# Optimization experiments

Measured on AMD Instinct MI355X. Metric: run time of the kernel, lower is better.

## Reference

```python
import jax, jax.numpy as jnp
import numpy as np

N_HEAD = 8
D_HEAD = 64
HIDDEN = 512
T = 2048
BS = 4
SCALE = D_HEAD ** -0.5


def setup_inputs() -> dict:
    key = jax.random.key(0)
    k1, k2, k3 = jax.random.split(key, 3)
    x = jax.random.normal(k1, (BS, T, HIDDEN), dtype=jnp.float32)
    # torch Linear weight is (out,in); we store as (in,out) for x @ W
    W_qkv = jax.random.normal(k2, (HIDDEN, (2 * N_HEAD + 1) * D_HEAD), dtype=jnp.float32) * 0.02
    W_out = jax.random.normal(k3, (D_HEAD, HIDDEN), dtype=jnp.float32) * 0.02
    return {"x": x, "W_qkv": W_qkv, "W_out": W_out}


def reference(x, W_qkv, W_out):
    bs, t, h = x.shape
    qkv = x @ W_qkv  # (bs, t, (2H+1)*d)
    q, k, v = jnp.split(qkv, [N_HEAD * D_HEAD, 2 * N_HEAD * D_HEAD], axis=-1)
    q = q.reshape(bs, t, N_HEAD, D_HEAD)
    k = k.reshape(bs, t, N_HEAD, D_HEAD)
    # v is shared across heads: (bs, t, d)
    score = jnp.einsum("bqhd,bkhd->bhqk", q, k) * SCALE
    causal = jnp.triu(jnp.full((t, t), -jnp.inf, dtype=score.dtype), 1)
    score = score + causal[None, None, :, :]
    prob = jax.nn.softmax(score, axis=-1)  # (bs, H, t, t)
    attn_vec = jnp.einsum("bhqk,bkd->bhqd", prob, v)  # shared V broadcast over heads
    m_attn_vec = jnp.mean(attn_vec, axis=1)  # head-mean: (bs, t, d)
    out = m_attn_vec @ W_out  # (bs, t, hidden)
    return out, attn_vec
```

## Files before the change

### kernel.cpp

```cpp
#include <hip/hip_runtime.h>
#include <hip/hip_bf16.h>

#define NHEAD  8
#define DHEAD  64
#define HIDDEN 512
#define SEQ_T  2048
#define BATCH  4
#define NQKV   1088
#define NT     32
#define NROWS  (BATCH * SEQ_T)
#define NBH    (BATCH * NHEAD)

typedef __attribute__((ext_vector_type(8))) short short8;
typedef __attribute__((ext_vector_type(4))) float f32x4;

__device__ __forceinline__ unsigned short f2bf(float f) {
  unsigned int u = __float_as_uint(f);
  u += 0x7FFFu + ((u >> 16) & 1u);
  return (unsigned short)(u >> 16);
}
__device__ __forceinline__ unsigned short f2bf_trunc(float f) {
  return (unsigned short)(__float_as_uint(f) >> 16);
}

__device__ __forceinline__ void load_lds16(const unsigned short* g, unsigned short* l) {
  __builtin_amdgcn_global_load_lds((const __attribute__((address_space(1))) void*)g,
                                   (__attribute__((address_space(3))) void*)l, 16, 0, 0);
}

#define DPPF(x, ctrl) \
  __int_as_float(__builtin_amdgcn_update_dpp(0, __float_as_int(x), (ctrl), 0xF, 0xF, true))
__device__ __forceinline__ float rsum16(float x) {
  x += DPPF(x, 0xB1);
  x += DPPF(x, 0x4E);
  x += DPPF(x, 0x141);
  x += DPPF(x, 0x140);
  return x;
}

__global__ __launch_bounds__(256) void cvt_x(const float* __restrict__ x,
                                             unsigned short* __restrict__ xb) {
  const size_t i0 = ((size_t)blockIdx.x * 256 + threadIdx.x) * 8;
  float4 a = *(const float4*)(x + i0);
  float4 b = *(const float4*)(x + i0 + 4);
  ushort4 u0, u1;
  u0.x = f2bf(a.x); u0.y = f2bf(a.y); u0.z = f2bf(a.z); u0.w = f2bf(a.w);
  u1.x = f2bf(b.x); u1.y = f2bf(b.y); u1.z = f2bf(b.z); u1.w = f2bf(b.w);
  *(ushort4*)(xb + i0) = u0;
  *(ushort4*)(xb + i0 + 4) = u1;
}

__global__ __launch_bounds__(256) void wt_bf16(const float* __restrict__ W,
                                               unsigned short* __restrict__ Wt) {
  const int n0 = blockIdx.x * 64;
  const int k0 = blockIdx.y * 64;
  const int tid = threadIdx.x;
  __shared__ float T[64 * 65];

#pragma unroll
  for (int i = 0; i < 4; ++i) {
    int f = tid + i * 256;
    int r = f >> 4;
    int c4 = (f & 15) * 4;
    float4 v = *(const float4*)(W + (size_t)(k0 + r) * NQKV + n0 + c4);
    T[r * 65 + c4 + 0] = v.x;
    T[r * 65 + c4 + 1] = v.y;
    T[r * 65 + c4 + 2] = v.z;
    T[r * 65 + c4 + 3] = v.w;
  }
  __syncthreads();

#pragma unroll
  for (int i = 0; i < 4; ++i) {
    int f = tid + i * 256;
    int n = f >> 4;
    int k4 = (f & 15) * 4;
    ushort4 u;
    u.x = f2bf(T[(k4 + 0) * 65 + n]);
    u.y = f2bf(T[(k4 + 1) * 65 + n]);
    u.z = f2bf(T[(k4 + 2) * 65 + n]);
    u.w = f2bf(T[(k4 + 3) * 65 + n]);
    *(ushort4*)(Wt + (size_t)(n0 + n) * HIDDEN + k0 + k4) = u;
  }
}

__global__ __launch_bounds__(256) void qkv_mfma(const unsigned short* __restrict__ Xb,
                                                const unsigned short* __restrict__ Wt,
                                                unsigned short* __restrict__ Y) {
  __shared__ __align__(16) unsigned short As[128 * 64];
  __shared__ __align__(16) unsigned short Bs[64 * 64];
  const int bm = blockIdx.x;
  const int bn = blockIdx.y;
  const int tid = threadIdx.x;
  const int wave = tid >> 6;
  const int lane = tid & 63;
  const int quad = lane >> 4;
  const int l15 = lane & 15;
  const int lrow = lane >> 3;
  const int lchunk = lane & 7;

  const unsigned short* xrow = Xb + (size_t)bm * 128 * HIDDEN;
  const unsigned short* wrow = Wt + (size_t)bn * 64 * HIDDEN;

  f32x4 acc[2][4];
#pragma unroll
  for (int mt = 0; mt < 2; ++mt)
#pragma unroll
    for (int nt = 0; nt < 4; ++nt) acc[mt][nt] = (f32x4){0.f, 0.f, 0.f, 0.f};

  for (int k0 = 0; k0 < HIDDEN; k0 += 64) {
    __syncthreads();
#pragma unroll
    for (int c = 0; c < 4; ++c) {
      int call = wave * 4 + c;
      int m = call * 8 + lrow;
      int clog = lchunk ^ lrow;
      load_lds16(xrow + (size_t)m * HIDDEN + k0 + clog * 8, &As[call * 512]);
    }
#pragma unroll
    for (int c = 0; c < 2; ++c) {
      int call = wave * 2 + c;
      int n = call * 8 + lrow;
      int clog = lchunk ^ lrow;
      load_lds16(wrow + (size_t)n * HIDDEN + k0 + clog * 8, &Bs[call * 512]);
    }
    __syncthreads();

#pragma unroll
    for (int ks = 0; ks < 2; ++ks) {
      short8 a[2], b[4];
#pragma unroll
      for (int mt = 0; mt < 2; ++mt) {
        int m = wave * 32 + mt * 16 + l15;
        int phys = (ks * 4 + quad) ^ (l15 & 7);
        a[mt] = *(const short8*)&As[m * 64 + phys * 8];
      }
#pragma unroll
      for (int nt = 0; nt < 4; ++nt) {
        int n = nt * 16 + l15;
        int phys = (ks * 4 + quad) ^ (l15 & 7);
        b[nt] = *(const short8*)&Bs[n * 64 + phys * 8];
      }
#pragma unroll
      for (int mt = 0; mt < 2; ++mt)
#pragma unroll
        for (int nt = 0; nt < 4; ++nt)
          acc[mt][nt] = __builtin_amdgcn_mfma_f32_16x16x32_bf16(a[mt], b[nt], acc[mt][nt], 0, 0, 0);
    }
  }

#pragma unroll
  for (int mt = 0; mt < 2; ++mt)
#pragma unroll
    for (int r = 0; r < 4; ++r) {
      int row = bm * 128 + wave * 32 + mt * 16 + quad * 4 + r;
#pragma unroll
      for (int nt = 0; nt < 4; ++nt) {
        int col = bn * 64 + nt * 16 + l15;
        Y[(size_t)row * NQKV + col] = f2bf(acc[mt][nt][r]);
      }
    }
}

__global__ __launch_bounds__(256) void v_transpose(const unsigned short* __restrict__ qkv,
                                                   unsigned short* __restrict__ vt) {
  const int b = blockIdx.x >> 5;
  const int k0 = (blockIdx.x & 31) * 64;
  const int tid = threadIdx.x;
  __shared__ unsigned short Vs[64 * 66];

#pragma unroll
  for (int i = 0; i < 8; ++i) {
    int c = tid + i * 256;
    int row = c >> 5;
    int col2 = c & 31;
    unsigned int v = *(const unsigned int*)(qkv + (size_t)(b * SEQ_T + k0 + row) * NQKV + 1024 + col2 * 2);
    *(unsigned int*)&Vs[row * 66 + col2 * 2] = v;
  }
  __syncthreads();

#pragma unroll
  for (int i = 0; i < 16; ++i) {
    int f = tid + i * 256;
    int d = f >> 6;
    int c = f & 63;
    vt[((size_t)b * DHEAD + d) * SEQ_T + k0 + c] = Vs[c * 66 + d];
  }
}

__global__ __launch_bounds__(256, 4) void attn_pass(const unsigned short* __restrict__ qkv,
                                                    const unsigned short* __restrict__ vt,
                                                    float* __restrict__ part0,
                                                    unsigned short* __restrict__ pbuf,
                                                    float* __restrict__ lbuf) {
  const int bh = blockIdx.x;
  const int y = blockIdx.y;
  const int qt = 15 - (y >> 1);
  const int kh = y & 1;
  const int b = bh >> 3;
  const int h = bh & 7;
  const int tid = threadIdx.x;
  const int wave = tid >> 6;
  const int lane = tid & 63;
  const int quad = lane >> 4;
  const int l15 = lane & 15;

  __shared__ __align__(16) unsigned short Ks[64 * 64];
  __shared__ __align__(16) unsigned short Vts[64 * 64];
  __shared__ __align__(16) unsigned short Ps[128 * 72];

  const unsigned short* bq = qkv + (size_t)b * SEQ_T * NQKV;
  const unsigned short* bvt = vt + (size_t)b * DHEAD * SEQ_T;
  const float SCl = 0.125f * 1.44269504f;

  const int q0 = qt * 128;
  const int kbeg = kh ? (qt + 1) : 0;
  const int kend = kh ? (2 * qt + 1) : qt;

  short8 aq[2][2];
#pragma unroll
  for (int s = 0; s < 2; ++s) {
    const unsigned short* qp = bq + (size_t)(q0 + s * 64 + wave * 16 + l15) * NQKV + h * 64 + quad * 8;
    aq[s][0] = *(const short8*)qp;
    aq[s][1] = *(const short8*)(qp + 32);
  }

  f32x4 o[2][4];
#pragma unroll
  for (int s = 0; s < 2; ++s)
#pragma unroll
    for (int t = 0; t < 4; ++t) o[s][t] = (f32x4){0.f, 0.f, 0.f, 0.f};
  float l_part[2][4] = {{0.f, 0.f, 0.f, 0.f}, {0.f, 0.f, 0.f, 0.f}};

  const int srow = tid >> 3;
  const int sch = (tid & 7) ^ (srow & 7);

  for (int kt = kbeg; kt <= kend; ++kt) {
    const int k0 = kt * 64;
    __syncthreads();
#pragma unroll
    for (int c = 0; c < 2; ++c) {
      load_lds16(bq + (size_t)(k0 + c * 32 + srow) * NQKV + 512 + h * 64 + sch * 8,
                 &Ks[c * 2048 + wave * 512]);
      load_lds16(bvt + (size_t)(c * 32 + srow) * SEQ_T + k0 + sch * 8,
                 &Vts[c * 2048 + wave * 512]);
    }
    __syncthreads();

    const bool needMask = (k0 + 63) > q0;

#pragma unroll
    for (int t = 0; t < 4; ++t) {
      const int n = l15 + 16 * t;
      const int ph0 = (quad ^ (l15 & 7)) * 8;
      short8 bk0 = *(const short8*)&Ks[n * 64 + ph0];
      short8 bk1 = *(const short8*)&Ks[n * 64 + (ph0 ^ 32)];
#pragma unroll
      for (int s = 0; s < 2; ++s) {
        f32x4 sv = (f32x4){0.f, 0.f, 0.f, 0.f};
        sv = __builtin_amdgcn_mfma_f32_16x16x32_bf16(aq[s][0], bk0, sv, 0, 0, 0);
        sv = __builtin_amdgcn_mfma_f32_16x16x32_bf16(aq[s][1], bk1, sv, 0, 0, 0);
        const int rbase = s * 64 + wave * 16 + quad * 4;
#pragma unroll
        for (int r = 0; r < 4; ++r) {
          float p = __builtin_amdgcn_exp2f(sv[r] * SCl);
          if (needMask) {
            int gcol = k0 + l15 + 16 * t;
            int grow = q0 + rbase + r;
            p = (gcol <= grow) ? p : 0.f;
          }
          l_part[s][r] += p;
          int prow = rbase + r;
          int colp = (l15 + 16 * t + ((prow >> 2) << 4)) & 63;
          Ps[prow * 72 + colp] = f2bf_trunc(p);
        }
      }
    }

    short8 ap[2][2];
#pragma unroll
    for (int s = 0; s < 2; ++s) {
      int prow = s * 64 + wave * 16 + l15;
      int rot = ((prow >> 2) << 1) & 7;
      int c0 = (quad + rot) & 7;
      int c1 = (quad + 4 + rot) & 7;
      ap[s][0] = *(const short8*)&Ps[prow * 72 + c0 * 8];
      ap[s][1] = *(const short8*)&Ps[prow * 72 + c1 * 8];
    }

#pragma unroll
    for (int t = 0; t < 4; ++t) {
      const int d = l15 + 16 * t;
      const int ph0 = (quad ^ (l15 & 7)) * 8;
      short8 bv0 = *(const short8*)&Vts[d * 64 + ph0];
      short8 bv1 = *(const short8*)&Vts[d * 64 + (ph0 ^ 32)];
#pragma unroll
      for (int s = 0; s < 2; ++s) {
        o[s][t] = __builtin_amdgcn_mfma_f32_16x16x32_bf16(ap[s][0], bv0, o[s][t], 0, 0, 0);
        o[s][t] = __builtin_amdgcn_mfma_f32_16x16x32_bf16(ap[s][1], bv1, o[s][t], 0, 0, 0);
      }
    }
  }

#pragma unroll
  for (int s = 0; s < 2; ++s) {
#pragma unroll
    for (int r = 0; r < 4; ++r) {
      float l = rsum16(l_part[s][r]);
      const int trow = q0 + s * 64 + wave * 16 + quad * 4 + r;
      if (l15 == 0) lbuf[kh * (NBH * SEQ_T) + bh * SEQ_T + trow] = l;
      const size_t base = ((size_t)bh * SEQ_T + trow) * DHEAD;
      if (kh == 0) {
#pragma unroll
        for (int t = 0; t < 4; ++t) part0[base + l15 + 16 * t] = o[s][t][r];
      } else {
#pragma unroll
        for (int t = 0; t < 4; ++t) pbuf[base + l15 + 16 * t] = f2bf(o[s][t][r]);
      }
    }
  }
}

__global__ __launch_bounds__(256) void merge_attn(float* __restrict__ attnv,
                                                  const unsigned short* __restrict__ pbuf,
                                                  const float* __restrict__ lbuf) {
  const int tid = threadIdx.x;
  const int row = blockIdx.x * 16 + (tid >> 4);
  const int d4 = (tid & 15) * 4;
  const float inv = 1.0f / (lbuf[row] + lbuf[NBH * SEQ_T + row]);
  const size_t idx = (size_t)row * DHEAD + d4;
  float4 A = *(const float4*)(attnv + idx);
  ushort4 B = *(const ushort4*)(pbuf + idx);
  float4 o;
  o.x = (A.x + __uint_as_float((unsigned int)B.x << 16)) * inv;
  o.y = (A.y + __uint_as_float((unsigned int)B.y << 16)) * inv;
  o.z = (A.z + __uint_as_float((unsigned int)B.z << 16)) * inv;
  o.w = (A.w + __uint_as_float((unsigned int)B.w << 16)) * inv;
  *(float4*)(attnv + idx) = o;
}

__global__ __launch_bounds__(256) void out_gemm(const float* __restrict__ attn,
                                                const float* __restrict__ Wout,
                                                float* __restrict__ out) {
  const int row0 = blockIdx.x * 16;
  const int tid = threadIdx.x;
  __shared__ float Ms[16][64];

#pragma unroll
  for (int i = 0; i < 4; ++i) {
    int f = tid + i * 256;
    int lr = f >> 6;
    int d = f & 63;
    int row = row0 + lr;
    int b = row >> 11;
    int t = row & 2047;
    float sum = 0.f;
#pragma unroll
    for (int hh = 0; hh < NHEAD; ++hh) {
      sum += attn[((size_t)(b * NHEAD + hh) * SEQ_T + t) * DHEAD + d];
    }
    Ms[lr][d] = sum * (1.0f / NHEAD);
  }
  __syncthreads();

  const int c0 = tid * 2;
  float a0[16], a1[16];
#pragma unroll
  for (int i = 0; i < 16; ++i) { a0[i] = 0.f; a1[i] = 0.f; }

  for (int d = 0; d < 64; ++d) {
    float2 w = *(const float2*)(Wout + (size_t)d * HIDDEN + c0);
#pragma unroll
    for (int lr = 0; lr < 16; ++lr) {
      float m = Ms[lr][d];
      a0[lr] += m * w.x;
      a1[lr] += m * w.y;
    }
  }
#pragma unroll
  for (int lr = 0; lr < 16; ++lr) {
    float2 v = make_float2(a0[lr], a1[lr]);
    *(float2*)(out + (size_t)(row0 + lr) * HIDDEN + c0) = v;
  }
}

extern "C" void kernel_launch(void* const* d_in, const int* in_sizes, int n_in,
                              void* d_out, int out_size, void* d_ws, size_t ws_size,
                              hipStream_t stream) {
  const float* x     = (const float*)d_in[0];
  const float* W_qkv = (const float*)d_in[1];
  const float* W_out = (const float*)d_in[2];

  float* out      = (float*)d_out;
  float* attn_vec = out + (size_t)BATCH * SEQ_T * HIDDEN;

  unsigned short* qkv = (unsigned short*)d_ws;
  unsigned short* vt  = qkv + (size_t)NROWS * NQKV;
  unsigned short* xb  = vt + (size_t)BATCH * DHEAD * SEQ_T;
  unsigned short* Wt  = xb + (size_t)NROWS * HIDDEN;
  unsigned short* pbuf = xb;
  float*          lbuf = (float*)Wt;

  cvt_x<<<dim3(NROWS * HIDDEN / (256 * 8)), 256, 0, stream>>>(x, xb);
  wt_bf16<<<dim3(17, 8), 256, 0, stream>>>(W_qkv, Wt);
  qkv_mfma<<<dim3(64, 17), 256, 0, stream>>>(xb, Wt, qkv);
  v_transpose<<<dim3(BATCH * NT), 256, 0, stream>>>(qkv, vt);
  attn_pass<<<dim3(NBH, 32), 256, 0, stream>>>(qkv, vt, attn_vec, pbuf, lbuf);
  merge_attn<<<dim3(NBH * SEQ_T / 16), 256, 0, stream>>>(attn_vec, pbuf, lbuf);
  out_gemm<<<dim3(512), 256, 0, stream>>>(attn_vec, W_out, out);
}
```

Measured before the change: 160.2 us.

## Pack P tile with perm writes via permuted V layout, prescale Q in GEMM

The softmax scale is folded into the QKV GEMM epilogue for the Q columns, which removes a multiply per score element in the attention loop. V is stored transposed with a permuted key order, so the P tile can be written as packed 64-bit stores built with byte-perm instead of scattered 16-bit stores and rotated reads. The attention loop is restructured to issue all QK MFMAs for a row group before the exponentials. The QKV GEMM also uses a 1D grid with a remapped block order for better L2 locality. The cost is that Q is rounded to bf16 after scaling and that the V layout now depends on this permutation.

```diff
diff --git a/kernel.cpp b/kernel.cpp
--- a/kernel.cpp
+++ b/kernel.cpp
@@ -10,6 +10,7 @@
 #define NT     32
 #define NROWS  (BATCH * SEQ_T)
 #define NBH    (BATCH * NHEAD)
+#define QSC    (0.125f * 1.44269504f)
 
 typedef __attribute__((ext_vector_type(8))) short short8;
 typedef __attribute__((ext_vector_type(4))) float f32x4;
@@ -18,9 +19,6 @@
   unsigned int u = __float_as_uint(f);
   u += 0x7FFFu + ((u >> 16) & 1u);
   return (unsigned short)(u >> 16);
-}
-__device__ __forceinline__ unsigned short f2bf_trunc(float f) {
-  return (unsigned short)(__float_as_uint(f) >> 16);
 }
 
 __device__ __forceinline__ void load_lds16(const unsigned short* g, unsigned short* l) {
@@ -89,8 +87,10 @@
                                                 unsigned short* __restrict__ Y) {
   __shared__ __align__(16) unsigned short As[128 * 64];
   __shared__ __align__(16) unsigned short Bs[64 * 64];
-  const int bm = blockIdx.x;
-  const int bn = blockIdx.y;
+  const int L = blockIdx.x;
+  const int slot = L >> 3;
+  const int bm = (L & 7) * 8 + (slot & 7);
+  const int bn = slot >> 3;
   const int tid = threadIdx.x;
   const int wave = tid >> 6;
   const int lane = tid & 63;
@@ -149,6 +149,7 @@
     }
   }
 
+  const float qs = (bn < 8) ? QSC : 1.0f;
 #pragma unroll
   for (int mt = 0; mt < 2; ++mt)
 #pragma unroll
@@ -157,7 +158,7 @@
 #pragma unroll
       for (int nt = 0; nt < 4; ++nt) {
         int col = bn * 64 + nt * 16 + l15;
-        Y[(size_t)row * NQKV + col] = f2bf(acc[mt][nt][r]);
+        Y[(size_t)row * NQKV + col] = f2bf(acc[mt][nt][r] * qs);
       }
     }
 }
@@ -183,8 +184,9 @@
   for (int i = 0; i < 16; ++i) {
     int f = tid + i * 256;
     int d = f >> 6;
-    int c = f & 63;
-    vt[((size_t)b * DHEAD + d) * SEQ_T + k0 + c] = Vs[c * 66 + d];
+    int n = f & 63;
+    int c = ((n & 3) << 4) | (n >> 2);
+    vt[((size_t)b * DHEAD + d) * SEQ_T + k0 + n] = Vs[c * 66 + d];
   }
 }
 
@@ -211,7 +213,6 @@
 
   const unsigned short* bq = qkv + (size_t)b * SEQ_T * NQKV;
   const unsigned short* bvt = vt + (size_t)b * DHEAD * SEQ_T;
-  const float SCl = 0.125f * 1.44269504f;
 
   const int q0 = qt * 128;
   const int kbeg = kh ? (qt + 1) : 0;
@@ -234,6 +235,7 @@
 
   const int srow = tid >> 3;
   const int sch = (tid & 7) ^ (srow & 7);
+  const int ph0 = (quad ^ (l15 & 7)) * 8;
 
   for (int kt = kbeg; kt <= kend; ++kt) {
     const int k0 = kt * 64;
@@ -249,57 +251,66 @@
 
     const bool needMask = (k0 + 63) > q0;
 
+    short8 bk[4][2];
 #pragma unroll
     for (int t = 0; t < 4; ++t) {
-      const int n = l15 + 16 * t;
-      const int ph0 = (quad ^ (l15 & 7)) * 8;
-      short8 bk0 = *(const short8*)&Ks[n * 64 + ph0];
-      short8 bk1 = *(const short8*)&Ks[n * 64 + (ph0 ^ 32)];
+      const unsigned short* kp = &Ks[(l15 + 16 * t) * 64];
+      bk[t][0] = *(const short8*)(kp + ph0);
+      bk[t][1] = *(const short8*)(kp + (ph0 ^ 32));
+    }
+
+#pragma unroll
+    for (int s = 0; s < 2; ++s) {
+      f32x4 pr[4];
+#pragma unroll
+      for (int t = 0; t < 4; ++t) {
+        f32x4 sv = (f32x4){0.f, 0.f, 0.f, 0.f};
+        sv = __builtin_amdgcn_mfma_f32_16x16x32_bf16(aq[s][0], bk[t][0], sv, 0, 0, 0);
+        sv = __builtin_amdgcn_mfma_f32_16x16x32_bf16(aq[s][1], bk[t][1], sv, 0, 0, 0);
+        pr[t] = sv;
+      }
+      const int rbase = s * 64 + wave * 16 + quad * 4;
+#pragma unroll
+      for (int t = 0; t < 4; ++t)
+#pragma unroll
+        for (int r = 0; r < 4; ++r) {
+          float p = __builtin_amdgcn_exp2f(pr[t][r]);
+          if (needMask)
+            p = (k0 + 16 * t + l15 <= q0 + rbase + r) ? p : 0.f;
+          l_part[s][r] += p;
+          pr[t][r] = p;
+        }
+#pragma unroll
+      for (int r = 0; r < 4; ++r) {
+        uint2 w;
+        w.x = __builtin_amdgcn_perm(__float_as_uint(pr[1][r]), __float_as_uint(pr[0][r]), 0x07060302u);
+        w.y = __builtin_amdgcn_perm(__float_as_uint(pr[3][r]), __float_as_uint(pr[2][r]), 0x07060302u);
+        *(uint2*)&Ps[(rbase + r) * 72 + 4 * l15] = w;
+      }
+    }
+
+    short8 bv[4][2];
+#pragma unroll
+    for (int t = 0; t < 4; ++t) {
+      const unsigned short* vp = &Vts[(l15 + 16 * t) * 64];
+      bv[t][0] = *(const short8*)(vp + ph0);
+      bv[t][1] = *(const short8*)(vp + (ph0 ^ 32));
+    }
+    short8 ap[2][2];
+#pragma unroll
+    for (int s = 0; s < 2; ++s) {
+      const unsigned short* pp = &Ps[(s * 64 + wave * 16 + l15) * 72];
+      ap[s][0] = *(const short8*)(pp + quad * 8);
+      ap[s][1] = *(const short8*)(pp + 32 + quad * 8);
+    }
+
+#pragma unroll
+    for (int t = 0; t < 4; ++t)
 #pragma unroll
       for (int s = 0; s < 2; ++s) {
-        f32x4 sv = (f32x4){0.f, 0.f, 0.f, 0.f};
-        sv = __builtin_amdgcn_mfma_f32_16x16x32_bf16(aq[s][0], bk0, sv, 0, 0, 0);
-        sv = __builtin_amdgcn_mfma_f32_16x16x32_bf16(aq[s][1], bk1, sv, 0, 0, 0);
-        const int rbase = s * 64 + wave * 16 + quad * 4;
-#pragma unroll
-        for (int r = 0; r < 4; ++r) {
-          float p = __builtin_amdgcn_exp2f(sv[r] * SCl);
-          if (needMask) {
-            int gcol = k0 + l15 + 16 * t;
-            int grow = q0 + rbase + r;
-            p = (gcol <= grow) ? p : 0.f;
-          }
-          l_part[s][r] += p;
-          int prow = rbase + r;
-          int colp = (l15 + 16 * t + ((prow >> 2) << 4)) & 63;
-          Ps[prow * 72 + colp] = f2bf_trunc(p);
-        }
-      }
-    }
-
-    short8 ap[2][2];
-#pragma unroll
-    for (int s = 0; s < 2; ++s) {
-      int prow = s * 64 + wave * 16 + l15;
-      int rot = ((prow >> 2) << 1) & 7;
-      int c0 = (quad + rot) & 7;
-      int c1 = (quad + 4 + rot) & 7;
-      ap[s][0] = *(const short8*)&Ps[prow * 72 + c0 * 8];
-      ap[s][1] = *(const short8*)&Ps[prow * 72 + c1 * 8];
-    }
-
-#pragma unroll
-    for (int t = 0; t < 4; ++t) {
-      const int d = l15 + 16 * t;
-      const int ph0 = (quad ^ (l15 & 7)) * 8;
-      short8 bv0 = *(const short8*)&Vts[d * 64 + ph0];
-      short8 bv1 = *(const short8*)&Vts[d * 64 + (ph0 ^ 32)];
-#pragma unroll
-      for (int s = 0; s < 2; ++s) {
-        o[s][t] = __builtin_amdgcn_mfma_f32_16x16x32_bf16(ap[s][0], bv0, o[s][t], 0, 0, 0);
-        o[s][t] = __builtin_amdgcn_mfma_f32_16x16x32_bf16(ap[s][1], bv1, o[s][t], 0, 0, 0);
-      }
-    }
+        o[s][t] = __builtin_amdgcn_mfma_f32_16x16x32_bf16(ap[s][0], bv[t][0], o[s][t], 0, 0, 0);
+        o[s][t] = __builtin_amdgcn_mfma_f32_16x16x32_bf16(ap[s][1], bv[t][1], o[s][t], 0, 0, 0);
+      }
   }
 
 #pragma unroll
@@ -403,7 +414,7 @@
 
   cvt_x<<<dim3(NROWS * HIDDEN / (256 * 8)), 256, 0, stream>>>(x, xb);
   wt_bf16<<<dim3(17, 8), 256, 0, stream>>>(W_qkv, Wt);
-  qkv_mfma<<<dim3(64, 17), 256, 0, stream>>>(xb, Wt, qkv);
+  qkv_mfma<<<dim3(64 * 17), 256, 0, stream>>>(xb, Wt, qkv);
   v_transpose<<<dim3(BATCH * NT), 256, 0, stream>>>(qkv, vt);
   attn_pass<<<dim3(NBH, 32), 256, 0, stream>>>(qkv, vt, attn_vec, pbuf, lbuf);
   merge_attn<<<dim3(NBH * SEQ_T / 16), 256, 0, stream>>>(attn_vec, pbuf, lbuf);
```

After: 155.4 us. -3.0%, faster.
